# Optimization experiments

Measured on AMD Instinct MI355X. Metric: run time of the kernel, lower is better.

Reference implementation:

```python
import jax, jax.numpy as jnp
import numpy as np

N, E, D_IN, D_H, D_OUT = 8000, 256000, 128, 128, 64
TEMP = 10.0       # config temperature.value (non-learnable)
WEIGHT = 1.0      # config weight.value (non-learnable)
LN_EPS = 1e-5


def _gcn_conv(x, W, b, src, dst, n):
    # PyG GCNConv: add self loops, sym-normalized aggregation, then bias.
    h = x @ W
    loop = jnp.arange(n)
    s = jnp.concatenate([src, loop])
    d = jnp.concatenate([dst, loop])
    deg = jnp.zeros((n,), h.dtype).at[d].add(1.0)
    dinv = jax.lax.rsqrt(jnp.maximum(deg, 1e-12))
    norm = dinv[s] * dinv[d]                       # [E+N]
    out = jax.ops.segment_sum(h[s] * norm[:, None], d, num_segments=n)
    return out + b


def _entropy_gradient(x, A, temperature, normalize):
    # E_i = 0.5 * sum_j A_ij ||x_i - x_j||^2  (dense adjacency, as in repo)
    sq = jnp.sum(x * x, axis=1)                    # [N]
    Ax = A @ x                                     # [N,d]
    deg = A.sum(axis=1)                            # [N]
    En = 0.5 * (deg * sq + A @ sq - 2.0 * jnp.sum(x * Ax, axis=1))
    if normalize:
        En = En / (jnp.max(En) + 1e-12)
    logits = -En / temperature
    P = jax.nn.softmax(logits)
    logP = jax.nn.log_softmax(logits)
    S = -jnp.sum(P * logP)
    c = P * (logP + S) / temperature               # dS/dE_k
    # dS/dx_i = c_i*(deg_i x_i - (Ax)_i) + (A^T c)_i x_i - (A^T (c*x))_i
    ATc = A.T @ c
    return (c[:, None] * (deg[:, None] * x - Ax)
            + ATc[:, None] * x - A.T @ (c[:, None] * x))


def _layer_norm(x, gamma, beta):
    mu = jnp.mean(x, axis=-1, keepdims=True)
    var = jnp.mean(jnp.square(x - mu), axis=-1, keepdims=True)
    return (x - mu) * jax.lax.rsqrt(var + LN_EPS) * gamma + beta


def setup_inputs() -> dict:
    key = jax.random.key(0)
    ks = jax.random.split(key, 6)
    def w(k, i, o):
        return jax.random.normal(k, (i, o), jnp.float32) / np.sqrt(i).astype(np.float32)
    return {
        "x": jax.random.normal(ks[0], (N, D_IN), jnp.float32),
        "edge_index": jax.random.randint(ks[1], (2, E), 0, N),
        "W1": w(ks[2], D_IN, D_H), "b1": jnp.zeros((D_H,), jnp.float32),
        "W2": w(ks[3], D_H, D_H), "b2": jnp.zeros((D_H,), jnp.float32),
        "W_out": w(ks[4], D_H, D_OUT), "b_out": jnp.zeros((D_OUT,), jnp.float32),
        "ln_gamma": jnp.ones((D_H,), jnp.float32),
        "ln_beta": jnp.zeros((D_H,), jnp.float32),
    }


def reference(x, edge_index, W1, b1, W2, b2, W_out, b_out, ln_gamma, ln_beta):
    n = x.shape[0]
    src, dst = edge_index[0], edge_index[1]
    # dense adjacency (to_dense_adj sums duplicate edges)
    A = jnp.zeros((n, n), x.dtype).at[src, dst].add(1.0)
    for W, b in ((W1, b1), (W2, b2)):
        h = _gcn_conv(x, W, b, src, dst, n)
        eg = jax.lax.stop_gradient(_entropy_gradient(h, A, TEMP, True))
        h = h + WEIGHT * eg
        h = jax.nn.relu(h)
        x = _layer_norm(h, ln_gamma, ln_beta)
    embedding = _gcn_conv(x, W_out, b_out, src, dst, n)
    return embedding
```

## Files before the change

### kernel.cpp

```cpp
#include <hip/hip_runtime.h>
#include <hip/hip_bf16.h>

#define DH 128

static constexpr float TEMP_ = 10.0f;
static constexpr float LN_EPS_ = 1e-5f;

__device__ __forceinline__ unsigned short f2bf(float f) {
  union { float f; unsigned int i; } v; v.f = f;
  unsigned int b = v.i + 0x7FFFu + ((v.i >> 16) & 1u);
  return (unsigned short)(b >> 16);
}
__device__ __forceinline__ void dec2(unsigned int u, float& lo, float& hi) {
  union { unsigned int i; float f; } a, b;
  a.i = u << 16; b.i = u & 0xFFFF0000u;
  lo = a.f; hi = b.f;
}
__device__ __forceinline__ void dec8(uint4 u, float* o) {
  dec2(u.x, o[0], o[1]); dec2(u.y, o[2], o[3]);
  dec2(u.z, o[4], o[5]); dec2(u.w, o[6], o[7]);
}
__device__ __forceinline__ unsigned int pack2(float lo, float hi) {
  return (unsigned int)f2bf(lo) | ((unsigned int)f2bf(hi) << 16);
}

__device__ __forceinline__ float grp_sum16(float v) {
  #pragma unroll
  for (int o = 8; o > 0; o >>= 1) v += __shfl_down(v, o, 16);
  return __shfl(v, 0, 16);
}

__device__ __forceinline__ float blkred(float v, bool mx, float* s4) {
  const int t = threadIdx.x;
  #pragma unroll
  for (int o = 32; o > 0; o >>= 1) {
    float u = __shfl_down(v, o, 64);
    v = mx ? fmaxf(v, u) : v + u;
  }
  __syncthreads();
  if ((t & 63) == 0) s4[t >> 6] = v;
  __syncthreads();
  float r = mx ? fmaxf(fmaxf(s4[0], s4[1]), fmaxf(s4[2], s4[3]))
               : (s4[0] + s4[1]) + (s4[2] + s4[3]);
  __syncthreads();
  return r;
}

__global__ void k_hist(const int* __restrict__ ei, int E, int* cnt_d, int* cnt_s) {
  for (int e = blockIdx.x * 256 + threadIdx.x; e < E; e += gridDim.x * 256) {
    atomicAdd(&cnt_s[ei[e]], 1);
    atomicAdd(&cnt_d[ei[E + e]], 1);
  }
}

__global__ __launch_bounds__(256) void k_scan_a(const int* __restrict__ cnt_d,
                                                const int* __restrict__ cnt_s,
                                                int* off_d, int* off_s, int* bsum,
                                                float* dinv, float* dego, int n) {
  __shared__ int ws4[4];
  const int t = threadIdx.x;
  const int dir = blockIdx.x >> 5, blk = blockIdx.x & 31;
  const int* cnt = dir ? cnt_s : cnt_d;
  int* off = dir ? off_s : off_d;
  const int NPB = (n + 31) >> 5;
  const int i = blk * NPB + t;
  const bool valid = (t < NPB) && (i < n);
  int tot = valid ? cnt[i] : 0;
  const int lane = t & 63, w = t >> 6;
  int v = tot;
  #pragma unroll
  for (int o = 1; o < 64; o <<= 1) {
    int u = __shfl_up(v, o, 64);
    if (lane >= o) v += u;
  }
  if (lane == 63) ws4[w] = v;
  __syncthreads();
  int wbase = 0;
  #pragma unroll
  for (int k = 0; k < 4; ++k) wbase += (k < w) ? ws4[k] : 0;
  const int excl = wbase + v - tot;
  if (valid) {
    off[i] = excl;
    if (dir == 0) dinv[i] = rsqrtf((float)tot + 1.0f);
    else          dego[i] = (float)tot;
  }
  if (t == 0) {
    int bt = 0;
    #pragma unroll
    for (int k = 0; k < 4; ++k) bt += ws4[k];
    bsum[dir * 32 + blk] = bt;
  }
}

__global__ __launch_bounds__(256) void k_scan_b(int* cnt_d, int* cnt_s,
                                                int* off_d, int* off_s,
                                                const int* __restrict__ bsum, int n) {
  __shared__ int sb;
  const int t = threadIdx.x;
  const int dir = blockIdx.x >> 5, blk = blockIdx.x & 31;
  int* cnt = dir ? cnt_s : cnt_d;
  int* off = dir ? off_s : off_d;
  if (t == 0) {
    int s = 0;
    for (int k = 0; k < blk; ++k) s += bsum[dir * 32 + k];
    sb = s;
  }
  __syncthreads();
  const int bbase = sb;
  const int NPB = (n + 31) >> 5;
  const int i = blk * NPB + t;
  if (t < NPB && i < n) {
    off[i] = bbase + off[i];
    cnt[i] = 0;
  }
  if (t == 1 && blk == 31) {
    int s = 0;
    for (int k = 0; k < 32; ++k) s += bsum[dir * 32 + k];
    off[n] = s;
  }
}

__global__ __launch_bounds__(256) void k_gemm1_fill(const float* __restrict__ X,
                                                    const float* __restrict__ W,
                                                    const float* __restrict__ dinv,
                                                    unsigned short* __restrict__ Hb,
                                                    const int* __restrict__ ei, int E,
                                                    const int* __restrict__ off_d,
                                                    const int* __restrict__ off_s,
                                                    int* cnt_d, int* cnt_s,
                                                    int* idx_d, int* idx_s, int NT) {
  __shared__ float Ws[64 * DH];
  __shared__ float xs[16 * 128];
  const int t = threadIdx.x;
  if ((int)blockIdx.x < NT) {
    const int row0 = blockIdx.x * 16;
    const float4* xg = (const float4*)(X + row0 * 128);
    float4* xs4 = (float4*)xs;
    xs4[t] = xg[t];
    xs4[t + 256] = xg[t + 256];
    const int c = t & 127, rg = t >> 7;
    float acc[8];
    #pragma unroll
    for (int r = 0; r < 8; ++r) acc[r] = 0.f;
    for (int kt = 0; kt < 2; ++kt) {
      __syncthreads();
      for (int i = t; i < 64 * DH; i += 256) Ws[i] = W[kt * 64 * DH + i];
      __syncthreads();
      for (int k = 0; k < 64; ++k) {
        float wv = Ws[k * DH + c];
        #pragma unroll
        for (int r = 0; r < 8; ++r)
          acc[r] += xs[(rg * 8 + r) * 128 + kt * 64 + k] * wv;
      }
    }
    #pragma unroll
    for (int r = 0; r < 8; ++r) {
      const int row = row0 + rg * 8 + r;
      Hb[row * DH + c] = f2bf(dinv[row] * acc[r]);
    }
  } else {
    const int nb = gridDim.x - NT;
    for (int e = (blockIdx.x - NT) * 256 + t; e < E; e += nb * 256) {
      int s = ei[e], d = ei[E + e];
      int p = atomicAdd(&cnt_d[d], 1);
      idx_d[off_d[d] + p] = s;
      int q = atomicAdd(&cnt_s[s], 1);
      idx_s[off_s[s] + q] = d;
    }
  }
}

__global__ __launch_bounds__(256) void k_conv_agg(const unsigned short* __restrict__ Hb,
                                                  const float* __restrict__ dinv,
                                                  const float* __restrict__ b,
                                                  const int* __restrict__ off_d,
                                                  const int* __restrict__ idx_d,
                                                  float* __restrict__ G,
                                                  unsigned short* __restrict__ Gb,
                                                  float* __restrict__ sq) {
  const int lane = threadIdx.x & 15;
  const int i = blockIdx.x * 16 + (threadIdx.x >> 4);
  const uint4* Hv = (const uint4*)Hb;
  const float di = dinv[i];
  float acc[8];
  dec8(Hv[i * 16 + lane], acc);
  int o = off_d[i];
  const int oe = off_d[i + 1];
  for (; o + 8 <= oe; o += 8) {
    int s[8]; uint4 r[8];
    #pragma unroll
    for (int j = 0; j < 8; ++j) s[j] = idx_d[o + j];
    #pragma unroll
    for (int j = 0; j < 8; ++j) r[j] = Hv[s[j] * 16 + lane];
    #pragma unroll
    for (int j = 0; j < 8; ++j) {
      float t8[8]; dec8(r[j], t8);
      #pragma unroll
      for (int k = 0; k < 8; ++k) acc[k] += t8[k];
    }
  }
  for (; o < oe; ++o) {
    int s = idx_d[o];
    float t8[8]; dec8(Hv[s * 16 + lane], t8);
    #pragma unroll
    for (int k = 0; k < 8; ++k) acc[k] += t8[k];
  }
  const float4 b0 = ((const float4*)b)[lane * 2];
  const float4 b1 = ((const float4*)b)[lane * 2 + 1];
  float gi[8];
  gi[0] = fmaf(di, acc[0], b0.x); gi[1] = fmaf(di, acc[1], b0.y);
  gi[2] = fmaf(di, acc[2], b0.z); gi[3] = fmaf(di, acc[3], b0.w);
  gi[4] = fmaf(di, acc[4], b1.x); gi[5] = fmaf(di, acc[5], b1.y);
  gi[6] = fmaf(di, acc[6], b1.z); gi[7] = fmaf(di, acc[7], b1.w);
  ((float4*)G)[i * 32 + lane * 2]     = make_float4(gi[0], gi[1], gi[2], gi[3]);
  ((float4*)G)[i * 32 + lane * 2 + 1] = make_float4(gi[4], gi[5], gi[6], gi[7]);
  uint4 gp;
  gp.x = pack2(gi[0], gi[1]); gp.y = pack2(gi[2], gi[3]);
  gp.z = pack2(gi[4], gi[5]); gp.w = pack2(gi[6], gi[7]);
  ((uint4*)Gb)[i * 16 + lane] = gp;
  float s2 = 0.f;
  #pragma unroll
  for (int k = 0; k < 8; ++k) s2 += gi[k] * gi[k];
  s2 = grp_sum16(s2);
  if (lane == 0) sq[i] = s2;
}

__global__ __launch_bounds__(256) void k_ax_en(const float* __restrict__ G,
                                               const unsigned short* __restrict__ Gb,
                                               const float* __restrict__ sq,
                                               const float* __restrict__ dego,
                                               const int* __restrict__ off_s,
                                               const int* __restrict__ idx_s,
                                               float* __restrict__ Ax,
                                               float* __restrict__ En) {
  const int lane = threadIdx.x & 15;
  const int i = blockIdx.x * 16 + (threadIdx.x >> 4);
  const uint4* Gv = (const uint4*)Gb;
  float axf[8];
  #pragma unroll
  for (int k = 0; k < 8; ++k) axf[k] = 0.f;
  float asq = 0.f;
  int o = off_s[i];
  const int oe = off_s[i + 1];
  for (; o + 8 <= oe; o += 8) {
    int s[8]; float qv[8]; uint4 r[8];
    #pragma unroll
    for (int j = 0; j < 8; ++j) s[j] = idx_s[o + j];
    #pragma unroll
    for (int j = 0; j < 8; ++j) { r[j] = Gv[s[j] * 16 + lane]; qv[j] = sq[s[j]]; }
    #pragma unroll
    for (int j = 0; j < 8; ++j) {
      float t8[8]; dec8(r[j], t8);
      asq += qv[j];
      #pragma unroll
      for (int k = 0; k < 8; ++k) axf[k] += t8[k];
    }
  }
  for (; o < oe; ++o) {
    int s = idx_s[o];
    float t8[8]; dec8(Gv[s * 16 + lane], t8);
    asq += sq[s];
    #pragma unroll
    for (int k = 0; k < 8; ++k) axf[k] += t8[k];
  }
  ((float4*)Ax)[i * 32 + lane * 2]     = make_float4(axf[0], axf[1], axf[2], axf[3]);
  ((float4*)Ax)[i * 32 + lane * 2 + 1] = make_float4(axf[4], axf[5], axf[6], axf[7]);
  const float4 g0 = ((const float4*)G)[i * 32 + lane * 2];
  const float4 g1 = ((const float4*)G)[i * 32 + lane * 2 + 1];
  float dot = g0.x * axf[0] + g0.y * axf[1] + g0.z * axf[2] + g0.w * axf[3]
            + g1.x * axf[4] + g1.y * axf[5] + g1.z * axf[6] + g1.w * axf[7];
  dot = grp_sum16(dot);
  if (lane == 0) En[i] = 0.5f * (dego[i] * sq[i] + asq - 2.f * dot);
}

template <int DOUT>
__global__ __launch_bounds__(256) void k_combine_gemm(const float* __restrict__ G,
                                                      const unsigned short* __restrict__ Gb,
                                                      const float* __restrict__ Ax,
                                                      const float* __restrict__ En,
                                                      const float* __restrict__ dego,
                                                      const float* __restrict__ dinv,
                                                      const int* __restrict__ off_d,
                                                      const int* __restrict__ idx_d,
                                                      const float* __restrict__ gamma,
                                                      const float* __restrict__ beta,
                                                      const float* __restrict__ W,
                                                      unsigned short* __restrict__ Hb,
                                                      int n) {
  __shared__ float Ws[64 * DOUT];
  __shared__ float xs[16 * 128];
  __shared__ float s4[4];
  const int t = threadIdx.x;
  float mloc = -3.0e38f;
  for (int k = t; k < n; k += 256) mloc = fmaxf(mloc, En[k]);
  const float m = blkred(mloc, true, s4);
  const float invden = -1.0f / ((m + 1e-12f) * TEMP_);
  float se = 0.f, sl = 0.f;
  for (int k = t; k < n; k += 256) {
    float li = En[k] * invden;
    float e = __expf(li);
    se += e; sl += e * li;
  }
  se = blkred(se, false, s4);
  sl = blkred(sl, false, s4);
  const float logZ = __logf(se);
  const float S = logZ - sl / se;
  const float cmul = (1.0f / se) * (1.0f / TEMP_);
  const float cadd = S - logZ;

  const int lane = t & 15;
  const int i = blockIdx.x * 16 + (t >> 4);
  const uint4* Gv = (const uint4*)Gb;
  const float4 g0 = ((const float4*)G)[i * 32 + lane * 2];
  const float4 g1 = ((const float4*)G)[i * 32 + lane * 2 + 1];
  const float gi[8] = { g0.x, g0.y, g0.z, g0.w, g1.x, g1.y, g1.z, g1.w };
  float tf[8];
  #pragma unroll
  for (int k = 0; k < 8; ++k) tf[k] = 0.f;
  float atc = 0.f;
  int o = off_d[i];
  const int oe = off_d[i + 1];
  for (; o + 8 <= oe; o += 8) {
    int s[8]; float ev[8]; uint4 r[8];
    #pragma unroll
    for (int j = 0; j < 8; ++j) s[j] = idx_d[o + j];
    #pragma unroll
    for (int j = 0; j < 8; ++j) { r[j] = Gv[s[j] * 16 + lane]; ev[j] = En[s[j]]; }
    #pragma unroll
    for (int j = 0; j < 8; ++j) {
      float ls = ev[j] * invden;
      float cs = __expf(ls) * cmul * (ls + cadd);
      atc += cs;
      float t8[8]; dec8(r[j], t8);
      #pragma unroll
      for (int k = 0; k < 8; ++k) tf[k] = fmaf(cs, t8[k], tf[k]);
    }
  }
  for (; o < oe; ++o) {
    int s = idx_d[o];
    float ls = En[s] * invden;
    float cs = __expf(ls) * cmul * (ls + cadd);
    atc += cs;
    float t8[8]; dec8(Gv[s * 16 + lane], t8);
    #pragma unroll
    for (int k = 0; k < 8; ++k) tf[k] = fmaf(cs, t8[k], tf[k]);
  }
  const float li_i = En[i] * invden;
  const float ci = __expf(li_i) * cmul * (li_i + cadd);
  const float dg = dego[i];
  const float4 a0 = ((const float4*)Ax)[i * 32 + lane * 2];
  const float4 a1 = ((const float4*)Ax)[i * 32 + lane * 2 + 1];
  const float axi[8] = { a0.x, a0.y, a0.z, a0.w, a1.x, a1.y, a1.z, a1.w };
  float v[8];
  float ssum = 0.f;
  #pragma unroll
  for (int k = 0; k < 8; ++k) {
    v[k] = fmaxf(gi[k] + ci * (dg * gi[k] - axi[k]) + atc * gi[k] - tf[k], 0.f);
    ssum += v[k];
  }
  float mu = grp_sum16(ssum) * (1.f / 128.f);
  float vsum = 0.f;
  #pragma unroll
  for (int k = 0; k < 8; ++k) {
    v[k] -= mu;
    vsum += v[k] * v[k];
  }
  float var = grp_sum16(vsum) * (1.f / 128.f);
  float rs = rsqrtf(var + LN_EPS_);
  const float4 ga0 = ((const float4*)gamma)[lane * 2];
  const float4 ga1 = ((const float4*)gamma)[lane * 2 + 1];
  const float4 be0 = ((const float4*)beta)[lane * 2];
  const float4 be1 = ((const float4*)beta)[lane * 2 + 1];
  float4 o0, o1;
  o0.x = fmaf(v[0] * rs, ga0.x, be0.x); o0.y = fmaf(v[1] * rs, ga0.y, be0.y);
  o0.z = fmaf(v[2] * rs, ga0.z, be0.z); o0.w = fmaf(v[3] * rs, ga0.w, be0.w);
  o1.x = fmaf(v[4] * rs, ga1.x, be1.x); o1.y = fmaf(v[5] * rs, ga1.y, be1.y);
  o1.z = fmaf(v[6] * rs, ga1.z, be1.z); o1.w = fmaf(v[7] * rs, ga1.w, be1.w);

  float* xrow = xs + (t >> 4) * 128 + lane * 8;
  ((float4*)xrow)[0] = o0;
  ((float4*)xrow)[1] = o1;

  const int row0 = blockIdx.x * 16;
  constexpr int RPT = (16 * DOUT) / 256;
  const int c = t % DOUT;
  const int rg = t / DOUT;
  float acc[RPT];
  #pragma unroll
  for (int r = 0; r < RPT; ++r) acc[r] = 0.f;
  for (int kt = 0; kt < 2; ++kt) {
    if (kt) __syncthreads();
    for (int idx = t; idx < 64 * DOUT; idx += 256) Ws[idx] = W[kt * 64 * DOUT + idx];
    __syncthreads();
    for (int k = 0; k < 64; ++k) {
      float wv = Ws[k * DOUT + c];
      #pragma unroll
      for (int r = 0; r < RPT; ++r)
        acc[r] += xs[(rg * RPT + r) * 128 + kt * 64 + k] * wv;
    }
  }
  #pragma unroll
  for (int r = 0; r < RPT; ++r) {
    const int row = row0 + rg * RPT + r;
    Hb[row * DOUT + c] = f2bf(dinv[row] * acc[r]);
  }
}

__global__ __launch_bounds__(256) void k_final_agg(const unsigned short* __restrict__ Hb,
                                                   const float* __restrict__ dinv,
                                                   const float* __restrict__ bout,
                                                   const int* __restrict__ off_d,
                                                   const int* __restrict__ idx_d,
                                                   float* __restrict__ out) {
  const int lane = threadIdx.x & 7;
  const int i = blockIdx.x * 32 + (threadIdx.x >> 3);
  const uint4* Hv = (const uint4*)Hb;
  const float di = dinv[i];
  float acc[8];
  dec8(Hv[i * 8 + lane], acc);
  int o = off_d[i];
  const int oe = off_d[i + 1];
  for (; o + 8 <= oe; o += 8) {
    int s[8]; uint4 r[8];
    #pragma unroll
    for (int j = 0; j < 8; ++j) s[j] = idx_d[o + j];
    #pragma unroll
    for (int j = 0; j < 8; ++j) r[j] = Hv[s[j] * 8 + lane];
    #pragma unroll
    for (int j = 0; j < 8; ++j) {
      float t8[8]; dec8(r[j], t8);
      #pragma unroll
      for (int k = 0; k < 8; ++k) acc[k] += t8[k];
    }
  }
  for (; o < oe; ++o) {
    int s = idx_d[o];
    float t8[8]; dec8(Hv[s * 8 + lane], t8);
    #pragma unroll
    for (int k = 0; k < 8; ++k) acc[k] += t8[k];
  }
  const float4 b0 = ((const float4*)bout)[lane * 2];
  const float4 b1 = ((const float4*)bout)[lane * 2 + 1];
  float4 r0, r1;
  r0.x = fmaf(di, acc[0], b0.x); r0.y = fmaf(di, acc[1], b0.y);
  r0.z = fmaf(di, acc[2], b0.z); r0.w = fmaf(di, acc[3], b0.w);
  r1.x = fmaf(di, acc[4], b1.x); r1.y = fmaf(di, acc[5], b1.y);
  r1.z = fmaf(di, acc[6], b1.z); r1.w = fmaf(di, acc[7], b1.w);
  ((float4*)out)[i * 16 + lane * 2]     = r0;
  ((float4*)out)[i * 16 + lane * 2 + 1] = r1;
}

extern "C" void kernel_launch(void* const* d_in, const int* in_sizes, int n_in,
                              void* d_out, int out_size, void* d_ws, size_t ws_size,
                              hipStream_t stream) {
  const float* x    = (const float*)d_in[0];
  const int*   ei   = (const int*)d_in[1];
  const float* W1   = (const float*)d_in[2];
  const float* b1   = (const float*)d_in[3];
  const float* W2   = (const float*)d_in[4];
  const float* b2   = (const float*)d_in[5];
  const float* Wout = (const float*)d_in[6];
  const float* bout = (const float*)d_in[7];
  const float* gam  = (const float*)d_in[8];
  const float* bet  = (const float*)d_in[9];
  float* out = (float*)d_out;

  const int N = in_sizes[0] / DH;
  const int E = in_sizes[1] / 2;

  float* ws = (float*)d_ws;
  float* G  = ws;   ws += N * DH;
  float* Ax = ws;   ws += N * DH;
  float* sq = ws;   ws += N;
  float* En = ws;   ws += N;
  float* dinv = ws; ws += N;
  float* dego = ws; ws += N;
  unsigned short* Hb = (unsigned short*)ws; ws += N * DH / 2;
  unsigned short* Gb = (unsigned short*)ws; ws += N * DH / 2;
  int* cnt_d  = (int*)ws; ws += N;
  int* cnt_s  = (int*)ws; ws += N;
  int* off_d  = (int*)ws; ws += N + 4;
  int* off_s  = (int*)ws; ws += N + 4;
  int* bsum   = (int*)ws; ws += 64;
  int* idx_d  = (int*)ws; ws += E;
  int* idx_s  = (int*)ws; ws += E;

  const int NT = N / 16;

  hipMemsetAsync(cnt_d, 0, 2 * N * sizeof(int), stream);
  k_hist<<<256, 256, 0, stream>>>(ei, E, cnt_d, cnt_s);
  k_scan_a<<<64, 256, 0, stream>>>(cnt_d, cnt_s, off_d, off_s, bsum, dinv, dego, N);
  k_scan_b<<<64, 256, 0, stream>>>(cnt_d, cnt_s, off_d, off_s, bsum, N);
  k_gemm1_fill<<<NT + (E + 255) / 256, 256, 0, stream>>>(x, W1, dinv, Hb, ei, E,
                                                         off_d, off_s, cnt_d, cnt_s,
                                                         idx_d, idx_s, NT);

  k_conv_agg<<<N / 16, 256, 0, stream>>>(Hb, dinv, b1, off_d, idx_d, G, Gb, sq);
  k_ax_en<<<N / 16, 256, 0, stream>>>(G, Gb, sq, dego, off_s, idx_s, Ax, En);
  k_combine_gemm<128><<<N / 16, 256, 0, stream>>>(G, Gb, Ax, En, dego, dinv, off_d,
                                                  idx_d, gam, bet, W2, Hb, N);
  k_conv_agg<<<N / 16, 256, 0, stream>>>(Hb, dinv, b2, off_d, idx_d, G, Gb, sq);
  k_ax_en<<<N / 16, 256, 0, stream>>>(G, Gb, sq, dego, off_s, idx_s, Ax, En);
  k_combine_gemm<64><<<N / 16, 256, 0, stream>>>(G, Gb, Ax, En, dego, dinv, off_d,
                                                 idx_d, gam, bet, Wout, Hb, N);
  k_final_agg<<<N / 32, 256, 0, stream>>>(Hb, dinv, bout, off_d, idx_d, out);
}
```

Measured before the change: 234.7 us.

## Fuse all stages into one persistent kernel with grid-wide barriers

Replaces the chain of about ten kernel launches with a single persistent kernel. Stages are separated by a software grid barrier built from atomics and fences, and each phase walks its tiles with grid-stride loops. The global max of the energy is now accumulated by an atomicMax in the energy phase instead of every block rescanning all of En. This removes launch gaps and redundant reductions, at the cost of barrier overhead, capped occupancy, and a deadlock risk if the sized grid is not fully co-resident.

```diff
diff --git a/kernel.cpp b/kernel.cpp
--- a/kernel.cpp
+++ b/kernel.cpp
@@ -1,5 +1,4 @@
 #include <hip/hip_runtime.h>
-#include <hip/hip_bf16.h>
 
 #define DH 128
 
@@ -46,258 +45,149 @@
   return r;
 }
 
-__global__ void k_hist(const int* __restrict__ ei, int E, int* cnt_d, int* cnt_s) {
-  for (int e = blockIdx.x * 256 + threadIdx.x; e < E; e += gridDim.x * 256) {
-    atomicAdd(&cnt_s[ei[e]], 1);
-    atomicAdd(&cnt_d[ei[E + e]], 1);
-  }
-}
-
-__global__ __launch_bounds__(256) void k_scan_a(const int* __restrict__ cnt_d,
-                                                const int* __restrict__ cnt_s,
-                                                int* off_d, int* off_s, int* bsum,
-                                                float* dinv, float* dego, int n) {
-  __shared__ int ws4[4];
+__device__ __forceinline__ void gsync(unsigned int* bar) {
+  __syncthreads();
+  if (threadIdx.x == 0) {
+    unsigned int* cnt = bar;
+    unsigned int* gen = bar + 1;
+    __builtin_amdgcn_fence(__ATOMIC_RELEASE, "agent");
+    unsigned int g = __hip_atomic_load(gen, __ATOMIC_RELAXED, __HIP_MEMORY_SCOPE_AGENT);
+    unsigned int a = __hip_atomic_fetch_add(cnt, 1u, __ATOMIC_RELAXED, __HIP_MEMORY_SCOPE_AGENT);
+    if (a == gridDim.x - 1u) {
+      __hip_atomic_store(cnt, 0u, __ATOMIC_RELAXED, __HIP_MEMORY_SCOPE_AGENT);
+      __hip_atomic_fetch_add(gen, 1u, __ATOMIC_RELEASE, __HIP_MEMORY_SCOPE_AGENT);
+    } else {
+      while (__hip_atomic_load(gen, __ATOMIC_RELAXED, __HIP_MEMORY_SCOPE_AGENT) == g)
+        __builtin_amdgcn_s_sleep(4);
+    }
+    __builtin_amdgcn_fence(__ATOMIC_ACQUIRE, "agent");
+  }
+  __syncthreads();
+}
+
+struct MP {
+  const float* x;
+  const int*   ei;
+  const float *W1, *b1, *W2, *b2, *Wout, *bout, *gam, *bet;
+  float* out;
+  float *G, *Ax, *sq, *En, *dinv, *dego, *gmax;
+  unsigned short *Hb, *Gb;
+  int *cnt_d, *cnt_s, *off_d, *off_s, *bsum, *idx_d, *idx_s;
+  unsigned int* bar;
+  int N, E;
+};
+
+__device__ __forceinline__ void conv_agg_phase(const MP& p, const float* b) {
   const int t = threadIdx.x;
-  const int dir = blockIdx.x >> 5, blk = blockIdx.x & 31;
-  const int* cnt = dir ? cnt_s : cnt_d;
-  int* off = dir ? off_s : off_d;
-  const int NPB = (n + 31) >> 5;
-  const int i = blk * NPB + t;
-  const bool valid = (t < NPB) && (i < n);
-  int tot = valid ? cnt[i] : 0;
-  const int lane = t & 63, w = t >> 6;
-  int v = tot;
-  #pragma unroll
-  for (int o = 1; o < 64; o <<= 1) {
-    int u = __shfl_up(v, o, 64);
-    if (lane >= o) v += u;
-  }
-  if (lane == 63) ws4[w] = v;
-  __syncthreads();
-  int wbase = 0;
-  #pragma unroll
-  for (int k = 0; k < 4; ++k) wbase += (k < w) ? ws4[k] : 0;
-  const int excl = wbase + v - tot;
-  if (valid) {
-    off[i] = excl;
-    if (dir == 0) dinv[i] = rsqrtf((float)tot + 1.0f);
-    else          dego[i] = (float)tot;
-  }
-  if (t == 0) {
-    int bt = 0;
-    #pragma unroll
-    for (int k = 0; k < 4; ++k) bt += ws4[k];
-    bsum[dir * 32 + blk] = bt;
-  }
-}
-
-__global__ __launch_bounds__(256) void k_scan_b(int* cnt_d, int* cnt_s,
-                                                int* off_d, int* off_s,
-                                                const int* __restrict__ bsum, int n) {
-  __shared__ int sb;
+  const int NT = p.N >> 4;
+  const uint4* Hv = (const uint4*)p.Hb;
+  for (int tile = blockIdx.x; tile < NT; tile += gridDim.x) {
+    const int lane = t & 15;
+    const int i = tile * 16 + (t >> 4);
+    const float di = p.dinv[i];
+    float acc[8];
+    dec8(Hv[i * 16 + lane], acc);
+    int o = p.off_d[i];
+    const int oe = p.off_d[i + 1];
+    for (; o + 8 <= oe; o += 8) {
+      int s[8]; uint4 r[8];
+      #pragma unroll
+      for (int j = 0; j < 8; ++j) s[j] = p.idx_d[o + j];
+      #pragma unroll
+      for (int j = 0; j < 8; ++j) r[j] = Hv[s[j] * 16 + lane];
+      #pragma unroll
+      for (int j = 0; j < 8; ++j) {
+        float t8[8]; dec8(r[j], t8);
+        #pragma unroll
+        for (int k = 0; k < 8; ++k) acc[k] += t8[k];
+      }
+    }
+    for (; o < oe; ++o) {
+      int s = p.idx_d[o];
+      float t8[8]; dec8(Hv[s * 16 + lane], t8);
+      #pragma unroll
+      for (int k = 0; k < 8; ++k) acc[k] += t8[k];
+    }
+    const float4 b0 = ((const float4*)b)[lane * 2];
+    const float4 b1 = ((const float4*)b)[lane * 2 + 1];
+    float gi[8];
+    gi[0] = fmaf(di, acc[0], b0.x); gi[1] = fmaf(di, acc[1], b0.y);
+    gi[2] = fmaf(di, acc[2], b0.z); gi[3] = fmaf(di, acc[3], b0.w);
+    gi[4] = fmaf(di, acc[4], b1.x); gi[5] = fmaf(di, acc[5], b1.y);
+    gi[6] = fmaf(di, acc[6], b1.z); gi[7] = fmaf(di, acc[7], b1.w);
+    ((float4*)p.G)[i * 32 + lane * 2]     = make_float4(gi[0], gi[1], gi[2], gi[3]);
+    ((float4*)p.G)[i * 32 + lane * 2 + 1] = make_float4(gi[4], gi[5], gi[6], gi[7]);
+    uint4 gp;
+    gp.x = pack2(gi[0], gi[1]); gp.y = pack2(gi[2], gi[3]);
+    gp.z = pack2(gi[4], gi[5]); gp.w = pack2(gi[6], gi[7]);
+    ((uint4*)p.Gb)[i * 16 + lane] = gp;
+    float s2 = 0.f;
+    #pragma unroll
+    for (int k = 0; k < 8; ++k) s2 += gi[k] * gi[k];
+    s2 = grp_sum16(s2);
+    if (lane == 0) p.sq[i] = s2;
+  }
+}
+
+__device__ __forceinline__ void ax_en_phase(const MP& p, float* gmax) {
   const int t = threadIdx.x;
-  const int dir = blockIdx.x >> 5, blk = blockIdx.x & 31;
-  int* cnt = dir ? cnt_s : cnt_d;
-  int* off = dir ? off_s : off_d;
-  if (t == 0) {
-    int s = 0;
-    for (int k = 0; k < blk; ++k) s += bsum[dir * 32 + k];
-    sb = s;
-  }
-  __syncthreads();
-  const int bbase = sb;
-  const int NPB = (n + 31) >> 5;
-  const int i = blk * NPB + t;
-  if (t < NPB && i < n) {
-    off[i] = bbase + off[i];
-    cnt[i] = 0;
-  }
-  if (t == 1 && blk == 31) {
-    int s = 0;
-    for (int k = 0; k < 32; ++k) s += bsum[dir * 32 + k];
-    off[n] = s;
-  }
-}
-
-__global__ __launch_bounds__(256) void k_gemm1_fill(const float* __restrict__ X,
-                                                    const float* __restrict__ W,
-                                                    const float* __restrict__ dinv,
-                                                    unsigned short* __restrict__ Hb,
-                                                    const int* __restrict__ ei, int E,
-                                                    const int* __restrict__ off_d,
-                                                    const int* __restrict__ off_s,
-                                                    int* cnt_d, int* cnt_s,
-                                                    int* idx_d, int* idx_s, int NT) {
-  __shared__ float Ws[64 * DH];
-  __shared__ float xs[16 * 128];
+  const int NT = p.N >> 4;
+  const uint4* Gv = (const uint4*)p.Gb;
+  for (int tile = blockIdx.x; tile < NT; tile += gridDim.x) {
+    const int lane = t & 15;
+    const int i = tile * 16 + (t >> 4);
+    float axf[8];
+    #pragma unroll
+    for (int k = 0; k < 8; ++k) axf[k] = 0.f;
+    float asq = 0.f;
+    int o = p.off_s[i];
+    const int oe = p.off_s[i + 1];
+    for (; o + 8 <= oe; o += 8) {
+      int s[8]; float qv[8]; uint4 r[8];
+      #pragma unroll
+      for (int j = 0; j < 8; ++j) s[j] = p.idx_s[o + j];
+      #pragma unroll
+      for (int j = 0; j < 8; ++j) { r[j] = Gv[s[j] * 16 + lane]; qv[j] = p.sq[s[j]]; }
+      #pragma unroll
+      for (int j = 0; j < 8; ++j) {
+        float t8[8]; dec8(r[j], t8);
+        asq += qv[j];
+        #pragma unroll
+        for (int k = 0; k < 8; ++k) axf[k] += t8[k];
+      }
+    }
+    for (; o < oe; ++o) {
+      int s = p.idx_s[o];
+      float t8[8]; dec8(Gv[s * 16 + lane], t8);
+      asq += p.sq[s];
+      #pragma unroll
+      for (int k = 0; k < 8; ++k) axf[k] += t8[k];
+    }
+    ((float4*)p.Ax)[i * 32 + lane * 2]     = make_float4(axf[0], axf[1], axf[2], axf[3]);
+    ((float4*)p.Ax)[i * 32 + lane * 2 + 1] = make_float4(axf[4], axf[5], axf[6], axf[7]);
+    const float4 g0 = ((const float4*)p.G)[i * 32 + lane * 2];
+    const float4 g1 = ((const float4*)p.G)[i * 32 + lane * 2 + 1];
+    float dot = g0.x * axf[0] + g0.y * axf[1] + g0.z * axf[2] + g0.w * axf[3]
+              + g1.x * axf[4] + g1.y * axf[5] + g1.z * axf[6] + g1.w * axf[7];
+    dot = grp_sum16(dot);
+    if (lane == 0) {
+      float en = 0.5f * (p.dego[i] * p.sq[i] + asq - 2.f * dot);
+      p.En[i] = en;
+      atomicMax((int*)gmax, __float_as_int(en));
+    }
+  }
+}
+
+template <int DOUT>
+__device__ __forceinline__ void combine_gemm_phase(const MP& p, const float* W,
+                                                   float m, float* Ws, float* xs,
+                                                   float* s4) {
   const int t = threadIdx.x;
-  if ((int)blockIdx.x < NT) {
-    const int row0 = blockIdx.x * 16;
-    const float4* xg = (const float4*)(X + row0 * 128);
-    float4* xs4 = (float4*)xs;
-    xs4[t] = xg[t];
-    xs4[t + 256] = xg[t + 256];
-    const int c = t & 127, rg = t >> 7;
-    float acc[8];
-    #pragma unroll
-    for (int r = 0; r < 8; ++r) acc[r] = 0.f;
-    for (int kt = 0; kt < 2; ++kt) {
-      __syncthreads();
-      for (int i = t; i < 64 * DH; i += 256) Ws[i] = W[kt * 64 * DH + i];
-      __syncthreads();
-      for (int k = 0; k < 64; ++k) {
-        float wv = Ws[k * DH + c];
-        #pragma unroll
-        for (int r = 0; r < 8; ++r)
-          acc[r] += xs[(rg * 8 + r) * 128 + kt * 64 + k] * wv;
-      }
-    }
-    #pragma unroll
-    for (int r = 0; r < 8; ++r) {
-      const int row = row0 + rg * 8 + r;
-      Hb[row * DH + c] = f2bf(dinv[row] * acc[r]);
-    }
-  } else {
-    const int nb = gridDim.x - NT;
-    for (int e = (blockIdx.x - NT) * 256 + t; e < E; e += nb * 256) {
-      int s = ei[e], d = ei[E + e];
-      int p = atomicAdd(&cnt_d[d], 1);
-      idx_d[off_d[d] + p] = s;
-      int q = atomicAdd(&cnt_s[s], 1);
-      idx_s[off_s[s] + q] = d;
-    }
-  }
-}
-
-__global__ __launch_bounds__(256) void k_conv_agg(const unsigned short* __restrict__ Hb,
-                                                  const float* __restrict__ dinv,
-                                                  const float* __restrict__ b,
-                                                  const int* __restrict__ off_d,
-                                                  const int* __restrict__ idx_d,
-                                                  float* __restrict__ G,
-                                                  unsigned short* __restrict__ Gb,
-                                                  float* __restrict__ sq) {
-  const int lane = threadIdx.x & 15;
-  const int i = blockIdx.x * 16 + (threadIdx.x >> 4);
-  const uint4* Hv = (const uint4*)Hb;
-  const float di = dinv[i];
-  float acc[8];
-  dec8(Hv[i * 16 + lane], acc);
-  int o = off_d[i];
-  const int oe = off_d[i + 1];
-  for (; o + 8 <= oe; o += 8) {
-    int s[8]; uint4 r[8];
-    #pragma unroll
-    for (int j = 0; j < 8; ++j) s[j] = idx_d[o + j];
-    #pragma unroll
-    for (int j = 0; j < 8; ++j) r[j] = Hv[s[j] * 16 + lane];
-    #pragma unroll
-    for (int j = 0; j < 8; ++j) {
-      float t8[8]; dec8(r[j], t8);
-      #pragma unroll
-      for (int k = 0; k < 8; ++k) acc[k] += t8[k];
-    }
-  }
-  for (; o < oe; ++o) {
-    int s = idx_d[o];
-    float t8[8]; dec8(Hv[s * 16 + lane], t8);
-    #pragma unroll
-    for (int k = 0; k < 8; ++k) acc[k] += t8[k];
-  }
-  const float4 b0 = ((const float4*)b)[lane * 2];
-  const float4 b1 = ((const float4*)b)[lane * 2 + 1];
-  float gi[8];
-  gi[0] = fmaf(di, acc[0], b0.x); gi[1] = fmaf(di, acc[1], b0.y);
-  gi[2] = fmaf(di, acc[2], b0.z); gi[3] = fmaf(di, acc[3], b0.w);
-  gi[4] = fmaf(di, acc[4], b1.x); gi[5] = fmaf(di, acc[5], b1.y);
-  gi[6] = fmaf(di, acc[6], b1.z); gi[7] = fmaf(di, acc[7], b1.w);
-  ((float4*)G)[i * 32 + lane * 2]     = make_float4(gi[0], gi[1], gi[2], gi[3]);
-  ((float4*)G)[i * 32 + lane * 2 + 1] = make_float4(gi[4], gi[5], gi[6], gi[7]);
-  uint4 gp;
-  gp.x = pack2(gi[0], gi[1]); gp.y = pack2(gi[2], gi[3]);
-  gp.z = pack2(gi[4], gi[5]); gp.w = pack2(gi[6], gi[7]);
-  ((uint4*)Gb)[i * 16 + lane] = gp;
-  float s2 = 0.f;
-  #pragma unroll
-  for (int k = 0; k < 8; ++k) s2 += gi[k] * gi[k];
-  s2 = grp_sum16(s2);
-  if (lane == 0) sq[i] = s2;
-}
-
-__global__ __launch_bounds__(256) void k_ax_en(const float* __restrict__ G,
-                                               const unsigned short* __restrict__ Gb,
-                                               const float* __restrict__ sq,
-                                               const float* __restrict__ dego,
-                                               const int* __restrict__ off_s,
-                                               const int* __restrict__ idx_s,
-                                               float* __restrict__ Ax,
-                                               float* __restrict__ En) {
-  const int lane = threadIdx.x & 15;
-  const int i = blockIdx.x * 16 + (threadIdx.x >> 4);
-  const uint4* Gv = (const uint4*)Gb;
-  float axf[8];
-  #pragma unroll
-  for (int k = 0; k < 8; ++k) axf[k] = 0.f;
-  float asq = 0.f;
-  int o = off_s[i];
-  const int oe = off_s[i + 1];
-  for (; o + 8 <= oe; o += 8) {
-    int s[8]; float qv[8]; uint4 r[8];
-    #pragma unroll
-    for (int j = 0; j < 8; ++j) s[j] = idx_s[o + j];
-    #pragma unroll
-    for (int j = 0; j < 8; ++j) { r[j] = Gv[s[j] * 16 + lane]; qv[j] = sq[s[j]]; }
-    #pragma unroll
-    for (int j = 0; j < 8; ++j) {
-      float t8[8]; dec8(r[j], t8);
-      asq += qv[j];
-      #pragma unroll
-      for (int k = 0; k < 8; ++k) axf[k] += t8[k];
-    }
-  }
-  for (; o < oe; ++o) {
-    int s = idx_s[o];
-    float t8[8]; dec8(Gv[s * 16 + lane], t8);
-    asq += sq[s];
-    #pragma unroll
-    for (int k = 0; k < 8; ++k) axf[k] += t8[k];
-  }
-  ((float4*)Ax)[i * 32 + lane * 2]     = make_float4(axf[0], axf[1], axf[2], axf[3]);
-  ((float4*)Ax)[i * 32 + lane * 2 + 1] = make_float4(axf[4], axf[5], axf[6], axf[7]);
-  const float4 g0 = ((const float4*)G)[i * 32 + lane * 2];
-  const float4 g1 = ((const float4*)G)[i * 32 + lane * 2 + 1];
-  float dot = g0.x * axf[0] + g0.y * axf[1] + g0.z * axf[2] + g0.w * axf[3]
-            + g1.x * axf[4] + g1.y * axf[5] + g1.z * axf[6] + g1.w * axf[7];
-  dot = grp_sum16(dot);
-  if (lane == 0) En[i] = 0.5f * (dego[i] * sq[i] + asq - 2.f * dot);
-}
-
-template <int DOUT>
-__global__ __launch_bounds__(256) void k_combine_gemm(const float* __restrict__ G,
-                                                      const unsigned short* __restrict__ Gb,
-                                                      const float* __restrict__ Ax,
-                                                      const float* __restrict__ En,
-                                                      const float* __restrict__ dego,
-                                                      const float* __restrict__ dinv,
-                                                      const int* __restrict__ off_d,
-                                                      const int* __restrict__ idx_d,
-                                                      const float* __restrict__ gamma,
-                                                      const float* __restrict__ beta,
-                                                      const float* __restrict__ W,
-                                                      unsigned short* __restrict__ Hb,
-                                                      int n) {
-  __shared__ float Ws[64 * DOUT];
-  __shared__ float xs[16 * 128];
-  __shared__ float s4[4];
-  const int t = threadIdx.x;
-  float mloc = -3.0e38f;
-  for (int k = t; k < n; k += 256) mloc = fmaxf(mloc, En[k]);
-  const float m = blkred(mloc, true, s4);
+  const int n = p.N;
   const float invden = -1.0f / ((m + 1e-12f) * TEMP_);
   float se = 0.f, sl = 0.f;
   for (int k = t; k < n; k += 256) {
-    float li = En[k] * invden;
+    float li = p.En[k] * invden;
     float e = __expf(li);
     se += e; sl += e * li;
   }
@@ -308,200 +198,326 @@
   const float cmul = (1.0f / se) * (1.0f / TEMP_);
   const float cadd = S - logZ;
 
-  const int lane = t & 15;
-  const int i = blockIdx.x * 16 + (t >> 4);
-  const uint4* Gv = (const uint4*)Gb;
-  const float4 g0 = ((const float4*)G)[i * 32 + lane * 2];
-  const float4 g1 = ((const float4*)G)[i * 32 + lane * 2 + 1];
-  const float gi[8] = { g0.x, g0.y, g0.z, g0.w, g1.x, g1.y, g1.z, g1.w };
-  float tf[8];
-  #pragma unroll
-  for (int k = 0; k < 8; ++k) tf[k] = 0.f;
-  float atc = 0.f;
-  int o = off_d[i];
-  const int oe = off_d[i + 1];
-  for (; o + 8 <= oe; o += 8) {
-    int s[8]; float ev[8]; uint4 r[8];
-    #pragma unroll
-    for (int j = 0; j < 8; ++j) s[j] = idx_d[o + j];
-    #pragma unroll
-    for (int j = 0; j < 8; ++j) { r[j] = Gv[s[j] * 16 + lane]; ev[j] = En[s[j]]; }
-    #pragma unroll
-    for (int j = 0; j < 8; ++j) {
-      float ls = ev[j] * invden;
+  const uint4* Gv = (const uint4*)p.Gb;
+  const int NT = n >> 4;
+  for (int tile = blockIdx.x; tile < NT; tile += gridDim.x) {
+    __syncthreads();
+    const int lane = t & 15;
+    const int i = tile * 16 + (t >> 4);
+    const float4 g0 = ((const float4*)p.G)[i * 32 + lane * 2];
+    const float4 g1 = ((const float4*)p.G)[i * 32 + lane * 2 + 1];
+    const float gi[8] = { g0.x, g0.y, g0.z, g0.w, g1.x, g1.y, g1.z, g1.w };
+    float tf[8];
+    #pragma unroll
+    for (int k = 0; k < 8; ++k) tf[k] = 0.f;
+    float atc = 0.f;
+    int o = p.off_d[i];
+    const int oe = p.off_d[i + 1];
+    for (; o + 8 <= oe; o += 8) {
+      int s[8]; float ev[8]; uint4 r[8];
+      #pragma unroll
+      for (int j = 0; j < 8; ++j) s[j] = p.idx_d[o + j];
+      #pragma unroll
+      for (int j = 0; j < 8; ++j) { r[j] = Gv[s[j] * 16 + lane]; ev[j] = p.En[s[j]]; }
+      #pragma unroll
+      for (int j = 0; j < 8; ++j) {
+        float ls = ev[j] * invden;
+        float cs = __expf(ls) * cmul * (ls + cadd);
+        atc += cs;
+        float t8[8]; dec8(r[j], t8);
+        #pragma unroll
+        for (int k = 0; k < 8; ++k) tf[k] = fmaf(cs, t8[k], tf[k]);
+      }
+    }
+    for (; o < oe; ++o) {
+      int s = p.idx_d[o];
+      float ls = p.En[s] * invden;
       float cs = __expf(ls) * cmul * (ls + cadd);
       atc += cs;
-      float t8[8]; dec8(r[j], t8);
+      float t8[8]; dec8(Gv[s * 16 + lane], t8);
       #pragma unroll
       for (int k = 0; k < 8; ++k) tf[k] = fmaf(cs, t8[k], tf[k]);
     }
-  }
-  for (; o < oe; ++o) {
-    int s = idx_d[o];
-    float ls = En[s] * invden;
-    float cs = __expf(ls) * cmul * (ls + cadd);
-    atc += cs;
-    float t8[8]; dec8(Gv[s * 16 + lane], t8);
-    #pragma unroll
-    for (int k = 0; k < 8; ++k) tf[k] = fmaf(cs, t8[k], tf[k]);
-  }
-  const float li_i = En[i] * invden;
-  const float ci = __expf(li_i) * cmul * (li_i + cadd);
-  const float dg = dego[i];
-  const float4 a0 = ((const float4*)Ax)[i * 32 + lane * 2];
-  const float4 a1 = ((const float4*)Ax)[i * 32 + lane * 2 + 1];
-  const float axi[8] = { a0.x, a0.y, a0.z, a0.w, a1.x, a1.y, a1.z, a1.w };
-  float v[8];
-  float ssum = 0.f;
-  #pragma unroll
-  for (int k = 0; k < 8; ++k) {
-    v[k] = fmaxf(gi[k] + ci * (dg * gi[k] - axi[k]) + atc * gi[k] - tf[k], 0.f);
-    ssum += v[k];
-  }
-  float mu = grp_sum16(ssum) * (1.f / 128.f);
-  float vsum = 0.f;
-  #pragma unroll
-  for (int k = 0; k < 8; ++k) {
-    v[k] -= mu;
-    vsum += v[k] * v[k];
-  }
-  float var = grp_sum16(vsum) * (1.f / 128.f);
-  float rs = rsqrtf(var + LN_EPS_);
-  const float4 ga0 = ((const float4*)gamma)[lane * 2];
-  const float4 ga1 = ((const float4*)gamma)[lane * 2 + 1];
-  const float4 be0 = ((const float4*)beta)[lane * 2];
-  const float4 be1 = ((const float4*)beta)[lane * 2 + 1];
-  float4 o0, o1;
-  o0.x = fmaf(v[0] * rs, ga0.x, be0.x); o0.y = fmaf(v[1] * rs, ga0.y, be0.y);
-  o0.z = fmaf(v[2] * rs, ga0.z, be0.z); o0.w = fmaf(v[3] * rs, ga0.w, be0.w);
-  o1.x = fmaf(v[4] * rs, ga1.x, be1.x); o1.y = fmaf(v[5] * rs, ga1.y, be1.y);
-  o1.z = fmaf(v[6] * rs, ga1.z, be1.z); o1.w = fmaf(v[7] * rs, ga1.w, be1.w);
-
-  float* xrow = xs + (t >> 4) * 128 + lane * 8;
-  ((float4*)xrow)[0] = o0;
-  ((float4*)xrow)[1] = o1;
-
-  const int row0 = blockIdx.x * 16;
-  constexpr int RPT = (16 * DOUT) / 256;
-  const int c = t % DOUT;
-  const int rg = t / DOUT;
-  float acc[RPT];
-  #pragma unroll
-  for (int r = 0; r < RPT; ++r) acc[r] = 0.f;
-  for (int kt = 0; kt < 2; ++kt) {
-    if (kt) __syncthreads();
-    for (int idx = t; idx < 64 * DOUT; idx += 256) Ws[idx] = W[kt * 64 * DOUT + idx];
+    const float li_i = p.En[i] * invden;
+    const float ci = __expf(li_i) * cmul * (li_i + cadd);
+    const float dg = p.dego[i];
+    const float4 a0 = ((const float4*)p.Ax)[i * 32 + lane * 2];
+    const float4 a1 = ((const float4*)p.Ax)[i * 32 + lane * 2 + 1];
+    const float axi[8] = { a0.x, a0.y, a0.z, a0.w, a1.x, a1.y, a1.z, a1.w };
+    float v[8];
+    float ssum = 0.f;
+    #pragma unroll
+    for (int k = 0; k < 8; ++k) {
+      v[k] = fmaxf(gi[k] + ci * (dg * gi[k] - axi[k]) + atc * gi[k] - tf[k], 0.f);
+      ssum += v[k];
+    }
+    float mu = grp_sum16(ssum) * (1.f / 128.f);
+    float vsum = 0.f;
+    #pragma unroll
+    for (int k = 0; k < 8; ++k) {
+      v[k] -= mu;
+      vsum += v[k] * v[k];
+    }
+    float var = grp_sum16(vsum) * (1.f / 128.f);
+    float rs = rsqrtf(var + LN_EPS_);
+    const float4 ga0 = ((const float4*)p.gam)[lane * 2];
+    const float4 ga1 = ((const float4*)p.gam)[lane * 2 + 1];
+    const float4 be0 = ((const float4*)p.bet)[lane * 2];
+    const float4 be1 = ((const float4*)p.bet)[lane * 2 + 1];
+    float4 o0, o1;
+    o0.x = fmaf(v[0] * rs, ga0.x, be0.x); o0.y = fmaf(v[1] * rs, ga0.y, be0.y);
+    o0.z = fmaf(v[2] * rs, ga0.z, be0.z); o0.w = fmaf(v[3] * rs, ga0.w, be0.w);
+    o1.x = fmaf(v[4] * rs, ga1.x, be1.x); o1.y = fmaf(v[5] * rs, ga1.y, be1.y);
+    o1.z = fmaf(v[6] * rs, ga1.z, be1.z); o1.w = fmaf(v[7] * rs, ga1.w, be1.w);
+
+    float* xrow = xs + (t >> 4) * 128 + lane * 8;
+    ((float4*)xrow)[0] = o0;
+    ((float4*)xrow)[1] = o1;
+
+    const int row0 = tile * 16;
+    constexpr int RPT = (16 * DOUT) / 256;
+    const int c = t % DOUT;
+    const int rg = t / DOUT;
+    float acc[RPT];
+    #pragma unroll
+    for (int r = 0; r < RPT; ++r) acc[r] = 0.f;
+    for (int kt = 0; kt < 2; ++kt) {
+      if (kt) __syncthreads();
+      for (int idx = t; idx < 64 * DOUT; idx += 256) Ws[idx] = W[kt * 64 * DOUT + idx];
+      __syncthreads();
+      for (int k = 0; k < 64; ++k) {
+        float wv = Ws[k * DOUT + c];
+        #pragma unroll
+        for (int r = 0; r < RPT; ++r)
+          acc[r] += xs[(rg * RPT + r) * 128 + kt * 64 + k] * wv;
+      }
+    }
+    #pragma unroll
+    for (int r = 0; r < RPT; ++r) {
+      const int row = row0 + rg * RPT + r;
+      p.Hb[row * DOUT + c] = f2bf(p.dinv[row] * acc[r]);
+    }
+  }
+}
+
+__device__ __forceinline__ void final_agg_phase(const MP& p) {
+  const int t = threadIdx.x;
+  const int NT32 = p.N >> 5;
+  const uint4* Hv = (const uint4*)p.Hb;
+  for (int tile = blockIdx.x; tile < NT32; tile += gridDim.x) {
+    const int lane = t & 7;
+    const int i = tile * 32 + (t >> 3);
+    const float di = p.dinv[i];
+    float acc[8];
+    dec8(Hv[i * 8 + lane], acc);
+    int o = p.off_d[i];
+    const int oe = p.off_d[i + 1];
+    for (; o + 8 <= oe; o += 8) {
+      int s[8]; uint4 r[8];
+      #pragma unroll
+      for (int j = 0; j < 8; ++j) s[j] = p.idx_d[o + j];
+      #pragma unroll
+      for (int j = 0; j < 8; ++j) r[j] = Hv[s[j] * 8 + lane];
+      #pragma unroll
+      for (int j = 0; j < 8; ++j) {
+        float t8[8]; dec8(r[j], t8);
+        #pragma unroll
+        for (int k = 0; k < 8; ++k) acc[k] += t8[k];
+      }
+    }
+    for (; o < oe; ++o) {
+      int s = p.idx_d[o];
+      float t8[8]; dec8(Hv[s * 8 + lane], t8);
+      #pragma unroll
+      for (int k = 0; k < 8; ++k) acc[k] += t8[k];
+    }
+    const float4 b0 = ((const float4*)p.bout)[lane * 2];
+    const float4 b1 = ((const float4*)p.bout)[lane * 2 + 1];
+    float4 r0, r1;
+    r0.x = fmaf(di, acc[0], b0.x); r0.y = fmaf(di, acc[1], b0.y);
+    r0.z = fmaf(di, acc[2], b0.z); r0.w = fmaf(di, acc[3], b0.w);
+    r1.x = fmaf(di, acc[4], b1.x); r1.y = fmaf(di, acc[5], b1.y);
+    r1.z = fmaf(di, acc[6], b1.z); r1.w = fmaf(di, acc[7], b1.w);
+    ((float4*)p.out)[i * 16 + lane * 2]     = r0;
+    ((float4*)p.out)[i * 16 + lane * 2 + 1] = r1;
+  }
+}
+
+__global__ __launch_bounds__(256, 2) void k_mega(MP p) {
+  __shared__ float Ws[64 * DH];
+  __shared__ float xs[16 * DH];
+  __shared__ float s4[4];
+  __shared__ int ws4[4];
+  const int t = threadIdx.x;
+  const int nb = gridDim.x;
+  const int N = p.N, E = p.E;
+  const int NT = N >> 4;
+
+  for (int e = blockIdx.x * 256 + t; e < E; e += nb * 256) {
+    atomicAdd(&p.cnt_s[p.ei[e]], 1);
+    atomicAdd(&p.cnt_d[p.ei[E + e]], 1);
+  }
+  gsync(p.bar);
+
+  if (blockIdx.x < 64) {
+    const int dir = blockIdx.x >> 5, blk = blockIdx.x & 31;
+    const int* cnt = dir ? p.cnt_s : p.cnt_d;
+    int* off = dir ? p.off_s : p.off_d;
+    const int NPB = (N + 31) >> 5;
+    const int i = blk * NPB + t;
+    const bool valid = (t < NPB) && (i < N);
+    int tot = valid ? cnt[i] : 0;
+    const int lane = t & 63, w = t >> 6;
+    int v = tot;
+    #pragma unroll
+    for (int o = 1; o < 64; o <<= 1) {
+      int u = __shfl_up(v, o, 64);
+      if (lane >= o) v += u;
+    }
+    if (lane == 63) ws4[w] = v;
     __syncthreads();
-    for (int k = 0; k < 64; ++k) {
-      float wv = Ws[k * DOUT + c];
-      #pragma unroll
-      for (int r = 0; r < RPT; ++r)
-        acc[r] += xs[(rg * RPT + r) * 128 + kt * 64 + k] * wv;
-    }
-  }
-  #pragma unroll
-  for (int r = 0; r < RPT; ++r) {
-    const int row = row0 + rg * RPT + r;
-    Hb[row * DOUT + c] = f2bf(dinv[row] * acc[r]);
-  }
-}
-
-__global__ __launch_bounds__(256) void k_final_agg(const unsigned short* __restrict__ Hb,
-                                                   const float* __restrict__ dinv,
-                                                   const float* __restrict__ bout,
-                                                   const int* __restrict__ off_d,
-                                                   const int* __restrict__ idx_d,
-                                                   float* __restrict__ out) {
-  const int lane = threadIdx.x & 7;
-  const int i = blockIdx.x * 32 + (threadIdx.x >> 3);
-  const uint4* Hv = (const uint4*)Hb;
-  const float di = dinv[i];
-  float acc[8];
-  dec8(Hv[i * 8 + lane], acc);
-  int o = off_d[i];
-  const int oe = off_d[i + 1];
-  for (; o + 8 <= oe; o += 8) {
-    int s[8]; uint4 r[8];
-    #pragma unroll
-    for (int j = 0; j < 8; ++j) s[j] = idx_d[o + j];
-    #pragma unroll
-    for (int j = 0; j < 8; ++j) r[j] = Hv[s[j] * 8 + lane];
-    #pragma unroll
-    for (int j = 0; j < 8; ++j) {
-      float t8[8]; dec8(r[j], t8);
-      #pragma unroll
-      for (int k = 0; k < 8; ++k) acc[k] += t8[k];
-    }
-  }
-  for (; o < oe; ++o) {
-    int s = idx_d[o];
-    float t8[8]; dec8(Hv[s * 8 + lane], t8);
-    #pragma unroll
-    for (int k = 0; k < 8; ++k) acc[k] += t8[k];
-  }
-  const float4 b0 = ((const float4*)bout)[lane * 2];
-  const float4 b1 = ((const float4*)bout)[lane * 2 + 1];
-  float4 r0, r1;
-  r0.x = fmaf(di, acc[0], b0.x); r0.y = fmaf(di, acc[1], b0.y);
-  r0.z = fmaf(di, acc[2], b0.z); r0.w = fmaf(di, acc[3], b0.w);
-  r1.x = fmaf(di, acc[4], b1.x); r1.y = fmaf(di, acc[5], b1.y);
-  r1.z = fmaf(di, acc[6], b1.z); r1.w = fmaf(di, acc[7], b1.w);
-  ((float4*)out)[i * 16 + lane * 2]     = r0;
-  ((float4*)out)[i * 16 + lane * 2 + 1] = r1;
+    int wbase = 0;
+    #pragma unroll
+    for (int k = 0; k < 4; ++k) wbase += (k < w) ? ws4[k] : 0;
+    const int excl = wbase + v - tot;
+    if (valid) {
+      off[i] = excl;
+      if (dir == 0) p.dinv[i] = rsqrtf((float)tot + 1.0f);
+      else          p.dego[i] = (float)tot;
+    }
+    if (t == 0) {
+      int bt = 0;
+      #pragma unroll
+      for (int k = 0; k < 4; ++k) bt += ws4[k];
+      p.bsum[dir * 32 + blk] = bt;
+    }
+  }
+  gsync(p.bar);
+
+  if (blockIdx.x < 64) {
+    const int dir = blockIdx.x >> 5, blk = blockIdx.x & 31;
+    int* cnt = dir ? p.cnt_s : p.cnt_d;
+    int* off = dir ? p.off_s : p.off_d;
+    if (t == 0) {
+      int s = 0;
+      for (int k = 0; k < blk; ++k) s += p.bsum[dir * 32 + k];
+      ws4[0] = s;
+    }
+    __syncthreads();
+    const int bbase = ws4[0];
+    const int NPB = (N + 31) >> 5;
+    const int i = blk * NPB + t;
+    if (t < NPB && i < N) {
+      off[i] = bbase + off[i];
+      cnt[i] = 0;
+    }
+    if (t == 1 && blk == 31) {
+      int s = 0;
+      for (int k = 0; k < 32; ++k) s += p.bsum[dir * 32 + k];
+      off[N] = s;
+    }
+  }
+  gsync(p.bar);
+
+  for (int tile = blockIdx.x; tile < NT; tile += nb) {
+    __syncthreads();
+    const int row0 = tile * 16;
+    const float4* xg = (const float4*)(p.x + row0 * DH);
+    float4* xs4 = (float4*)xs;
+    xs4[t] = xg[t];
+    xs4[t + 256] = xg[t + 256];
+    const int c = t & 127, rg = t >> 7;
+    float acc[8];
+    #pragma unroll
+    for (int r = 0; r < 8; ++r) acc[r] = 0.f;
+    for (int kt = 0; kt < 2; ++kt) {
+      __syncthreads();
+      for (int i2 = t; i2 < 64 * DH; i2 += 256) Ws[i2] = p.W1[kt * 64 * DH + i2];
+      __syncthreads();
+      for (int k = 0; k < 64; ++k) {
+        float wv = Ws[k * DH + c];
+        #pragma unroll
+        for (int r = 0; r < 8; ++r)
+          acc[r] += xs[(rg * 8 + r) * DH + kt * 64 + k] * wv;
+      }
+    }
+    #pragma unroll
+    for (int r = 0; r < 8; ++r) {
+      const int row = row0 + rg * 8 + r;
+      p.Hb[row * DH + c] = f2bf(p.dinv[row] * acc[r]);
+    }
+  }
+  for (int e = blockIdx.x * 256 + t; e < E; e += nb * 256) {
+    int s = p.ei[e], d = p.ei[E + e];
+    int pp = atomicAdd(&p.cnt_d[d], 1);
+    p.idx_d[p.off_d[d] + pp] = s;
+    int q = atomicAdd(&p.cnt_s[s], 1);
+    p.idx_s[p.off_s[s] + q] = d;
+  }
+  gsync(p.bar);
+
+  conv_agg_phase(p, p.b1);
+  gsync(p.bar);
+  ax_en_phase(p, p.gmax);
+  gsync(p.bar);
+  combine_gemm_phase<DH>(p, p.W2, p.gmax[0], Ws, xs, s4);
+  gsync(p.bar);
+
+  conv_agg_phase(p, p.b2);
+  gsync(p.bar);
+  ax_en_phase(p, p.gmax + 1);
+  gsync(p.bar);
+  combine_gemm_phase<64>(p, p.Wout, p.gmax[1], Ws, xs, s4);
+  gsync(p.bar);
+
+  final_agg_phase(p);
 }
 
 extern "C" void kernel_launch(void* const* d_in, const int* in_sizes, int n_in,
                               void* d_out, int out_size, void* d_ws, size_t ws_size,
                               hipStream_t stream) {
-  const float* x    = (const float*)d_in[0];
-  const int*   ei   = (const int*)d_in[1];
-  const float* W1   = (const float*)d_in[2];
-  const float* b1   = (const float*)d_in[3];
-  const float* W2   = (const float*)d_in[4];
-  const float* b2   = (const float*)d_in[5];
-  const float* Wout = (const float*)d_in[6];
-  const float* bout = (const float*)d_in[7];
-  const float* gam  = (const float*)d_in[8];
-  const float* bet  = (const float*)d_in[9];
-  float* out = (float*)d_out;
+  MP p;
+  p.x    = (const float*)d_in[0];
+  p.ei   = (const int*)d_in[1];
+  p.W1   = (const float*)d_in[2];
+  p.b1   = (const float*)d_in[3];
+  p.W2   = (const float*)d_in[4];
+  p.b2   = (const float*)d_in[5];
+  p.Wout = (const float*)d_in[6];
+  p.bout = (const float*)d_in[7];
+  p.gam  = (const float*)d_in[8];
+  p.bet  = (const float*)d_in[9];
+  p.out  = (float*)d_out;
 
   const int N = in_sizes[0] / DH;
   const int E = in_sizes[1] / 2;
+  p.N = N; p.E = E;
 
   float* ws = (float*)d_ws;
-  float* G  = ws;   ws += N * DH;
-  float* Ax = ws;   ws += N * DH;
-  float* sq = ws;   ws += N;
-  float* En = ws;   ws += N;
-  float* dinv = ws; ws += N;
-  float* dego = ws; ws += N;
-  unsigned short* Hb = (unsigned short*)ws; ws += N * DH / 2;
-  unsigned short* Gb = (unsigned short*)ws; ws += N * DH / 2;
-  int* cnt_d  = (int*)ws; ws += N;
-  int* cnt_s  = (int*)ws; ws += N;
-  int* off_d  = (int*)ws; ws += N + 4;
-  int* off_s  = (int*)ws; ws += N + 4;
-  int* bsum   = (int*)ws; ws += 64;
-  int* idx_d  = (int*)ws; ws += E;
-  int* idx_s  = (int*)ws; ws += E;
-
-  const int NT = N / 16;
-
-  hipMemsetAsync(cnt_d, 0, 2 * N * sizeof(int), stream);
-  k_hist<<<256, 256, 0, stream>>>(ei, E, cnt_d, cnt_s);
-  k_scan_a<<<64, 256, 0, stream>>>(cnt_d, cnt_s, off_d, off_s, bsum, dinv, dego, N);
-  k_scan_b<<<64, 256, 0, stream>>>(cnt_d, cnt_s, off_d, off_s, bsum, N);
-  k_gemm1_fill<<<NT + (E + 255) / 256, 256, 0, stream>>>(x, W1, dinv, Hb, ei, E,
-                                                         off_d, off_s, cnt_d, cnt_s,
-                                                         idx_d, idx_s, NT);
-
-  k_conv_agg<<<N / 16, 256, 0, stream>>>(Hb, dinv, b1, off_d, idx_d, G, Gb, sq);
-  k_ax_en<<<N / 16, 256, 0, stream>>>(G, Gb, sq, dego, off_s, idx_s, Ax, En);
-  k_combine_gemm<128><<<N / 16, 256, 0, stream>>>(G, Gb, Ax, En, dego, dinv, off_d,
-                                                  idx_d, gam, bet, W2, Hb, N);
-  k_conv_agg<<<N / 16, 256, 0, stream>>>(Hb, dinv, b2, off_d, idx_d, G, Gb, sq);
-  k_ax_en<<<N / 16, 256, 0, stream>>>(G, Gb, sq, dego, off_s, idx_s, Ax, En);
-  k_combine_gemm<64><<<N / 16, 256, 0, stream>>>(G, Gb, Ax, En, dego, dinv, off_d,
-                                                 idx_d, gam, bet, Wout, Hb, N);
-  k_final_agg<<<N / 32, 256, 0, stream>>>(Hb, dinv, bout, off_d, idx_d, out);
-}
+  p.G  = ws;   ws += N * DH;
+  p.Ax = ws;   ws += N * DH;
+  p.sq = ws;   ws += N;
+  p.En = ws;   ws += N;
+  p.dinv = ws; ws += N;
+  p.dego = ws; ws += N;
+  p.Hb = (unsigned short*)ws; ws += N * DH / 2;
+  p.Gb = (unsigned short*)ws; ws += N * DH / 2;
+  p.cnt_d = (int*)ws; ws += N;
+  p.cnt_s = (int*)ws; ws += N;
+  p.gmax  = (float*)ws; ws += 2;
+  p.bar   = (unsigned int*)ws; ws += 2;
+  p.off_d = (int*)ws; ws += N + 4;
+  p.off_s = (int*)ws; ws += N + 4;
+  p.bsum  = (int*)ws; ws += 64;
+  p.idx_d = (int*)ws; ws += E;
+  p.idx_s = (int*)ws; ws += E;
+
+  int mb = 0;
+  if (hipOccupancyMaxActiveBlocksPerMultiprocessor(&mb, k_mega, 256, 0) != hipSuccess)
+    mb = 0;
+  int nb = (mb > 0) ? mb * 256 : 64;
+  if (nb > 1024) nb = 1024;
+
+  hipMemsetAsync(p.cnt_d, 0, (size_t)(2 * N + 4) * sizeof(int), stream);
+  k_mega<<<nb, 256, 0, stream>>>(p);
+}
```

New measurement: 590.1 us. 151% more time.
